# Performance work log

Hardware: AMD Instinct MI355X
Metric: run time of the kernel (lower is better)

## Reference

```python
import jax, jax.numpy as jnp
import numpy as np

NUM_USERS = 100000
NUM_ITEMS = 50000
EMBED_K = 64
N_EDGES = 2000000
N_NODES = NUM_USERS + NUM_ITEMS


def setup_inputs() -> dict:
    key = jax.random.key(0)
    k1, k2, k3, k4, k5 = jax.random.split(key, 5)
    # xavier_normal for [N, K]: std = sqrt(2 / (N + K)); use a simple small std
    def xav(k, n, d):
        std = np.sqrt(2.0 / (n + d)).astype(np.float32)
        return jax.random.normal(k, (n, d), dtype=jnp.float32) * std
    Gu = xav(k1, NUM_USERS, EMBED_K)
    Gi = xav(k2, NUM_ITEMS, EMBED_K)
    Gut = xav(k3, NUM_USERS, EMBED_K)
    Git = xav(k4, NUM_ITEMS, EMBED_K)
    edge_index = jax.random.randint(k5, (2, N_EDGES), 0, N_NODES, dtype=jnp.int32)
    return {"Gu": Gu, "Gi": Gi, "Gut": Gut, "Git": Git,
            "edge_index": edge_index, "n_layers": 3}


def reference(Gu, Gi, Gut, Git, edge_index, n_layers):
    n_nodes = Gu.shape[0] + Gi.shape[0]
    src, dst = edge_index[0], edge_index[1]
    # symmetric gcn normalization: 1/sqrt(deg_src * deg_dst)
    ones = jnp.ones(src.shape[0], dtype=Gu.dtype)
    deg = jax.ops.segment_sum(ones, dst, num_segments=n_nodes)
    deg = jnp.maximum(deg, 1.0)
    norm = jax.lax.rsqrt(deg[src] * deg[dst])  # [E]

    def prop(x):  # x: [N, K] -> [N, K]
        msg = x[src] * norm[:, None]           # [E, K] gather
        return jax.ops.segment_sum(msg, dst, num_segments=n_nodes)

    alpha = jnp.asarray([1.0 / (k + 1) for k in range(n_layers + 1)], dtype=Gu.dtype)

    def run(x0):
        out = alpha[0] * x0
        x = x0
        for k in range(n_layers):
            x = prop(x)
            out = out + alpha[k + 1] * x
        return out

    collab = run(jnp.concatenate([Gu, Gi], axis=0))   # LGConv stack
    textual = run(jnp.concatenate([Gut, Git], axis=0))  # NodeNodeTextLayer stack
    return collab + textual  # [N_NODES, K]
```

## Files before the change

### kernel.cpp

```cpp
#include <hip/hip_runtime.h>
#include <hip/hip_fp16.h>

#define KD 64
#define NPC 1024
#define TILE 2048

__device__ __forceinline__ float h2f(unsigned short u) {
    return __half2float(__ushort_as_half(u));
}
__device__ __forceinline__ unsigned short f2h(float f) {
    return __half_as_ushort(__float2half(f));
}


__global__ void bhist_kernel(const int* __restrict__ dst, int* __restrict__ cntb,
                             int E, int NBC) {
    extern __shared__ int lcnt[];
    for (int i = threadIdx.x; i < NBC; i += blockDim.x) lcnt[i] = 0;
    __syncthreads();
    for (int i = blockIdx.x * blockDim.x + threadIdx.x; i < E; i += gridDim.x * blockDim.x)
        atomicAdd(&lcnt[dst[i] >> 10], 1);
    __syncthreads();
    for (int i = threadIdx.x; i < NBC; i += blockDim.x) {
        int v = lcnt[i];
        if (v) atomicAdd(&cntb[i], v);
    }
}

__global__ void scan_small_kernel(const int* __restrict__ cnt, int* __restrict__ bptr,
                                  int* __restrict__ cursor, int n, int E) {
    __shared__ int s[256];
    int t = threadIdx.x;
    int v = (t < n) ? cnt[t] : 0;
    s[t] = v;
    __syncthreads();
    for (int off = 1; off < 256; off <<= 1) {
        int add = (t >= off) ? s[t - off] : 0;
        __syncthreads();
        s[t] += add;
        __syncthreads();
    }
    int excl = s[t] - v;
    if (t < n) { bptr[t] = excl; cursor[t] = excl; }
    if (t == 0) bptr[n] = E;
}


__global__ __launch_bounds__(256)
void csplit_kernel(const int* __restrict__ src, const int* __restrict__ dst,
                   int* __restrict__ cursor, unsigned int* __restrict__ staged,
                   int E, int NBC, int ntiles) {
    __shared__ unsigned int  ord[TILE];
    __shared__ unsigned short obkt[TILE];
    __shared__ int hist[256];
    __shared__ int lofs[256];
    __shared__ int gbase[256];
    int tid = threadIdx.x;

    for (int tile = blockIdx.x; tile < ntiles; tile += gridDim.x) {
        int e0 = tile * TILE;
        int n = E - e0; if (n > TILE) n = TILE;

        if (tid < NBC) hist[tid] = 0;
        __syncthreads();
        for (int i = tid; i < n; i += 256)
            atomicAdd(&hist[dst[e0 + i] >> 10], 1);
        __syncthreads();
        int v = (tid < NBC) ? hist[tid] : 0;
        lofs[tid] = v;
        __syncthreads();
        for (int off = 1; off < 256; off <<= 1) {
            int add = (tid >= off) ? lofs[tid - off] : 0;
            __syncthreads();
            lofs[tid] += add;
            __syncthreads();
        }
        int excl = lofs[tid] - v;
        lofs[tid] = excl;
        if (tid < NBC) {
            gbase[tid] = atomicAdd(&cursor[tid], v);
            hist[tid] = 0;
        }
        __syncthreads();
        for (int i = tid; i < n; i += 256) {
            int dd = dst[e0 + i];
            int ss = src[e0 + i];
            int b = dd >> 10;
            int p = lofs[b] + atomicAdd(&hist[b], 1);
            ord[p] = (unsigned int)ss | (((unsigned int)dd & 1023u) << 18);
            obkt[p] = (unsigned short)b;
        }
        __syncthreads();
        for (int i = tid; i < n; i += 256) {
            int b = obkt[i];
            staged[gbase[b] + (i - lofs[b])] = ord[i];
        }
        __syncthreads();
    }
}


__global__ __launch_bounds__(1024)
void csort_kernel(const unsigned int* __restrict__ staged, const int* __restrict__ bptr,
                  int* __restrict__ sorted_src, int2* __restrict__ rowinfo,
                  float* __restrict__ r, float* __restrict__ rinv,
                  int n_nodes, int E) {
    __shared__ int cnt[NPC];
    __shared__ int s[NPC];
    __shared__ int lofs[NPC];
    int b = blockIdx.x;
    int tid = threadIdx.x;
    int begin = bptr[b], end = bptr[b + 1];

    cnt[tid] = 0;
    __syncthreads();
    for (int i = begin + tid; i < end; i += 1024)
        atomicAdd(&cnt[(staged[i] >> 18) & 1023u], 1);
    __syncthreads();
    int v = cnt[tid];
    s[tid] = v;
    __syncthreads();
    for (int off = 1; off < 1024; off <<= 1) {
        int add = (tid >= off) ? s[tid - off] : 0;
        __syncthreads();
        s[tid] += add;
        __syncthreads();
    }
    int excl = s[tid] - v;
    lofs[tid] = excl;
    int node = b * NPC + tid;
    if (node < n_nodes) {
        float d = fmaxf((float)v, 1.0f);
        rowinfo[node] = make_int2(begin + excl, v);
        r[node] = rsqrtf(d);
        rinv[node] = sqrtf(d);
    }
    cnt[tid] = 0;
    __syncthreads();
    for (int i = begin + tid; i < end; i += 1024) {
        unsigned int u = staged[i];
        int ld = (u >> 18) & 1023u;
        int p = begin + lofs[ld] + atomicAdd(&cnt[ld], 1);
        sorted_src[p] = (int)(u & 0x3FFFFu);
    }
}


__global__ void combine_kernel(const float4* __restrict__ Gu, const float4* __restrict__ Gi,
                               const float4* __restrict__ Gut, const float4* __restrict__ Git,
                               const float* __restrict__ r,
                               ushort4* __restrict__ xs,
                               int nu4, int total4) {
    for (int i = blockIdx.x * blockDim.x + threadIdx.x; i < total4; i += gridDim.x * blockDim.x) {
        float4 a, b;
        if (i < nu4) { a = Gu[i]; b = Gut[i]; }
        else         { a = Gi[i - nu4]; b = Git[i - nu4]; }
        float rr = r[i >> 4];
        ushort4 p;
        p.x = f2h((a.x + b.x) * rr); p.y = f2h((a.y + b.y) * rr);
        p.z = f2h((a.z + b.z) * rr); p.w = f2h((a.w + b.w) * rr);
        xs[i] = p;
    }
}

__global__ __launch_bounds__(256)
void gather_kernel(const int2* __restrict__ rowinfo, const int* __restrict__ sorted_src,
                   const float* __restrict__ r, const uint2* __restrict__ xs,
                   ushort4* __restrict__ xs_next,
                   const float4* __restrict__ Gu, const float4* __restrict__ Gi,
                   const float4* __restrict__ Gut, const float4* __restrict__ Git,
                   const float* __restrict__ rinv,
                   const ushort4* __restrict__ xs1, const ushort4* __restrict__ xs2,
                   float4* __restrict__ out, int nu, int N, int zrow, int last) {
    int wid = (blockIdx.x * blockDim.x + threadIdx.x) >> 6;
    int lane = threadIdx.x & 63;
    int n0 = wid * 2;
    int n1 = n0 + 1;
    if (n0 >= N) return;
    int2 ri0 = rowinfo[n0];
    int2 ri1 = (n1 < N) ? rowinfo[n1] : make_int2(0, 0);
    int sub = lane >> 4;
    int li  = lane & 15;

    float ax0 = 0.f, ay0 = 0.f, az0 = 0.f, aw0 = 0.f;
    float ax1 = 0.f, ay1 = 0.f, az1 = 0.f, aw1 = 0.f;
    int maxy = ri0.y > ri1.y ? ri0.y : ri1.y;

    for (int boff = 0; boff < maxy; boff += 64) {
        int nb0 = ri0.y - boff; nb0 = nb0 < 0 ? 0 : (nb0 > 64 ? 64 : nb0);
        int nb1 = ri1.y - boff; nb1 = nb1 < 0 ? 0 : (nb1 > 64 ? 64 : nb1);
        int es0 = 0, es1 = 0;
        if (nb0 > 0) {
            int e = ri0.x + boff + lane;
            int laste = ri0.x + ri0.y - 1;
            es0 = sorted_src[e > laste ? laste : e];
        }
        if (nb1 > 0) {
            int e = ri1.x + boff + lane;
            int laste = ri1.x + ri1.y - 1;
            es1 = sorted_src[e > laste ? laste : e];
        }
        int nbm = nb0 > nb1 ? nb0 : nb1;
        for (int c = 0; c < nbm; c += 16) {
            int j0 = c + sub * 4;
            int t0 = __shfl(es0, j0 + 0);
            int t1 = __shfl(es0, j0 + 1);
            int t2 = __shfl(es0, j0 + 2);
            int t3 = __shfl(es0, j0 + 3);
            int q0 = __shfl(es1, j0 + 0);
            int q1 = __shfl(es1, j0 + 1);
            int q2 = __shfl(es1, j0 + 2);
            int q3 = __shfl(es1, j0 + 3);
            t0 = (j0     < nb0) ? t0 : zrow;
            t1 = (j0 + 1 < nb0) ? t1 : zrow;
            t2 = (j0 + 2 < nb0) ? t2 : zrow;
            t3 = (j0 + 3 < nb0) ? t3 : zrow;
            q0 = (j0     < nb1) ? q0 : zrow;
            q1 = (j0 + 1 < nb1) ? q1 : zrow;
            q2 = (j0 + 2 < nb1) ? q2 : zrow;
            q3 = (j0 + 3 < nb1) ? q3 : zrow;
            uint2 w0 = xs[t0 * 16 + li];
            uint2 w1 = xs[t1 * 16 + li];
            uint2 w2 = xs[t2 * 16 + li];
            uint2 w3 = xs[t3 * 16 + li];
            uint2 v0 = xs[q0 * 16 + li];
            uint2 v1 = xs[q1 * 16 + li];
            uint2 v2 = xs[q2 * 16 + li];
            uint2 v3 = xs[q3 * 16 + li];
            {
                __half2 sa = __hadd2(__hadd2(__builtin_bit_cast(__half2, w0.x),
                                             __builtin_bit_cast(__half2, w1.x)),
                                     __hadd2(__builtin_bit_cast(__half2, w2.x),
                                             __builtin_bit_cast(__half2, w3.x)));
                __half2 sb = __hadd2(__hadd2(__builtin_bit_cast(__half2, w0.y),
                                             __builtin_bit_cast(__half2, w1.y)),
                                     __hadd2(__builtin_bit_cast(__half2, w2.y),
                                             __builtin_bit_cast(__half2, w3.y)));
                float2 fa = __half22float2(sa);
                float2 fb = __half22float2(sb);
                ax0 += fa.x; ay0 += fa.y; az0 += fb.x; aw0 += fb.y;
            }
            {
                __half2 sa = __hadd2(__hadd2(__builtin_bit_cast(__half2, v0.x),
                                             __builtin_bit_cast(__half2, v1.x)),
                                     __hadd2(__builtin_bit_cast(__half2, v2.x),
                                             __builtin_bit_cast(__half2, v3.x)));
                __half2 sb = __hadd2(__hadd2(__builtin_bit_cast(__half2, v0.y),
                                             __builtin_bit_cast(__half2, v1.y)),
                                     __hadd2(__builtin_bit_cast(__half2, v2.y),
                                             __builtin_bit_cast(__half2, v3.y)));
                float2 fa = __half22float2(sa);
                float2 fb = __half22float2(sb);
                ax1 += fa.x; ay1 += fa.y; az1 += fb.x; aw1 += fb.y;
            }
        }
    }
    ax0 += __shfl_xor(ax0, 16); ay0 += __shfl_xor(ay0, 16);
    az0 += __shfl_xor(az0, 16); aw0 += __shfl_xor(aw0, 16);
    ax1 += __shfl_xor(ax1, 16); ay1 += __shfl_xor(ay1, 16);
    az1 += __shfl_xor(az1, 16); aw1 += __shfl_xor(aw1, 16);
    ax0 += __shfl_xor(ax0, 32); ay0 += __shfl_xor(ay0, 32);
    az0 += __shfl_xor(az0, 32); aw0 += __shfl_xor(aw0, 32);
    ax1 += __shfl_xor(ax1, 32); ay1 += __shfl_xor(ay1, 32);
    az1 += __shfl_xor(az1, 32); aw1 += __shfl_xor(aw1, 32);

    int node = (lane < 16) ? n0 : n1;
    int lli  = lane & 15;
    if (lane < 32 && node < N) {
        float sx = (lane < 16) ? ax0 : ax1;
        float sy = (lane < 16) ? ay0 : ay1;
        float sz = (lane < 16) ? az0 : az1;
        float sw = (lane < 16) ? aw0 : aw1;
        float rr = r[node];
        int idx = node * 16 + lli;
        if (!last) {
            float s = rr * rr;
            ushort4 p;
            p.x = f2h(sx * s); p.y = f2h(sy * s);
            p.z = f2h(sz * s); p.w = f2h(sw * s);
            xs_next[idx] = p;
        } else {
            const float a1 = 0.5f, a2 = 1.0f / 3.0f, a3 = 0.25f;
            float4 a, b;
            if (node < nu) { a = Gu[idx]; b = Gut[idx]; }
            else           { int j = idx - nu * 16; a = Gi[j]; b = Git[j]; }
            float rv = rinv[node];
            ushort4 u1 = xs1[idx];
            ushort4 u2 = xs2[idx];
            float4 o;
            o.x = a.x + b.x + rv * (a1 * h2f(u1.x) + a2 * h2f(u2.x)) + a3 * (sx * rr);
            o.y = a.y + b.y + rv * (a1 * h2f(u1.y) + a2 * h2f(u2.y)) + a3 * (sy * rr);
            o.z = a.z + b.z + rv * (a1 * h2f(u1.z) + a2 * h2f(u2.z)) + a3 * (sz * rr);
            o.w = a.w + b.w + rv * (a1 * h2f(u1.w) + a2 * h2f(u2.w)) + a3 * (sw * rr);
            out[idx] = o;
        }
    }
}


extern "C" void kernel_launch(void* const* d_in, const int* in_sizes, int n_in,
                              void* d_out, int out_size, void* d_ws, size_t ws_size,
                              hipStream_t stream) {
    const float* Gu  = (const float*)d_in[0];
    const float* Gi  = (const float*)d_in[1];
    const float* Gut = (const float*)d_in[2];
    const float* Git = (const float*)d_in[3];
    const int*   edge_index = (const int*)d_in[4];

    const int nuK = in_sizes[0];
    const int niK = in_sizes[1];
    const int n_nodes = (nuK + niK) / KD;
    const int E = in_sizes[4] / 2;
    const int totalK = nuK + niK;
    const int total4 = totalK / 4;
    const int nu4 = nuK / 4;
    const int nu = nuK / KD;
    const int NBC = (n_nodes + NPC - 1) / NPC;
    const int ntiles = (E + TILE - 1) / TILE;

    const int* src = edge_index;
    const int* dst = edge_index + E;

    auto align_up = [](size_t v) { return (v + 255) & ~(size_t)255; };
    char* ws = (char*)d_ws;
    size_t off = 0;
    int*          cntb       = (int*)(ws + off);          off += align_up((size_t)NBC * 4);
    int*          bptr       = (int*)(ws + off);          off += align_up((size_t)(NBC + 1) * 4);
    int*          cursor     = (int*)(ws + off);          off += align_up((size_t)NBC * 4);
    int2*         rowinfo    = (int2*)(ws + off);         off += align_up((size_t)n_nodes * 8);
    float*        r          = (float*)(ws + off);        off += align_up((size_t)n_nodes * 4);
    float*        rinv       = (float*)(ws + off);        off += align_up((size_t)n_nodes * 4);
    unsigned int* staged     = (unsigned int*)(ws + off); off += align_up((size_t)E * 4);
    int*          sorted_src = (int*)(ws + off);          off += align_up((size_t)E * 4);
    unsigned short* xs0      = (unsigned short*)(ws + off); off += align_up(((size_t)totalK + KD) * 2);
    unsigned short* xs1      = (unsigned short*)(ws + off); off += align_up(((size_t)totalK + KD) * 2);
    unsigned short* xs2      = (unsigned short*)(ws + off); off += align_up(((size_t)totalK + KD) * 2);
    if (off > ws_size) return;

    float* out = (float*)d_out;

    const int BLK = 256;
    const int grid_v = 2048;
    const int n_waves = (n_nodes + 1) / 2;
    const int grid_g = ((size_t)n_waves * 64 + BLK - 1) / BLK;
    const int zrow = n_nodes;

    hipMemsetAsync(cntb, 0, (size_t)NBC * 4, stream);
    hipMemsetAsync(xs0 + (size_t)n_nodes * KD, 0, KD * 2, stream);
    hipMemsetAsync(xs1 + (size_t)n_nodes * KD, 0, KD * 2, stream);
    hipMemsetAsync(xs2 + (size_t)n_nodes * KD, 0, KD * 2, stream);

    bhist_kernel<<<256, BLK, (size_t)NBC * 4, stream>>>(dst, cntb, E, NBC);
    scan_small_kernel<<<1, 256, 0, stream>>>(cntb, bptr, cursor, NBC, E);
    csplit_kernel<<<ntiles, BLK, 0, stream>>>(src, dst, cursor, staged, E, NBC, ntiles);
    csort_kernel<<<NBC, 1024, 0, stream>>>(staged, bptr, sorted_src, rowinfo, r, rinv,
                                           n_nodes, E);

    combine_kernel<<<grid_v, BLK, 0, stream>>>((const float4*)Gu, (const float4*)Gi,
                                               (const float4*)Gut, (const float4*)Git,
                                               r, (ushort4*)xs0, nu4, total4);

    gather_kernel<<<grid_g, BLK, 0, stream>>>(rowinfo, sorted_src, r,
                                              (const uint2*)xs0, (ushort4*)xs1,
                                              nullptr, nullptr, nullptr, nullptr,
                                              nullptr, nullptr, nullptr, nullptr,
                                              nu, n_nodes, zrow, 0);
    gather_kernel<<<grid_g, BLK, 0, stream>>>(rowinfo, sorted_src, r,
                                              (const uint2*)xs1, (ushort4*)xs2,
                                              nullptr, nullptr, nullptr, nullptr,
                                              nullptr, nullptr, nullptr, nullptr,
                                              nu, n_nodes, zrow, 0);
    gather_kernel<<<grid_g, BLK, 0, stream>>>(rowinfo, sorted_src, r,
                                              (const uint2*)xs2, nullptr,
                                              (const float4*)Gu, (const float4*)Gi,
                                              (const float4*)Gut, (const float4*)Git,
                                              rinv, (const ushort4*)xs1,
                                              (const ushort4*)xs2,
                                              (float4*)out, nu, n_nodes, zrow, 1);
}
```

Baseline: 230.6 us.

## Map four nodes per wavefront with one 16-lane group per node in gather

The gather kernel now gives each wavefront four destination nodes, each served by one 16-lane group that reads its own 16 neighbor ids per step, instead of two nodes spread across all four subgroups. This removes the cross-subgroup shuffle reductions at the end and halves the number of waves launched. In exchange each wave runs to the longest of four degrees rather than two, so divergence from imbalanced degrees may grow. Each group still issues four gathers per inner step.

```diff
diff --git a/kernel.cpp b/kernel.cpp
--- a/kernel.cpp
+++ b/kernel.cpp
@@ -174,110 +174,56 @@
                    float4* __restrict__ out, int nu, int N, int zrow, int last) {
     int wid = (blockIdx.x * blockDim.x + threadIdx.x) >> 6;
     int lane = threadIdx.x & 63;
-    int n0 = wid * 2;
-    int n1 = n0 + 1;
-    if (n0 >= N) return;
-    int2 ri0 = rowinfo[n0];
-    int2 ri1 = (n1 < N) ? rowinfo[n1] : make_int2(0, 0);
     int sub = lane >> 4;
     int li  = lane & 15;
-
-    float ax0 = 0.f, ay0 = 0.f, az0 = 0.f, aw0 = 0.f;
-    float ax1 = 0.f, ay1 = 0.f, az1 = 0.f, aw1 = 0.f;
-    int maxy = ri0.y > ri1.y ? ri0.y : ri1.y;
-
-    for (int boff = 0; boff < maxy; boff += 64) {
-        int nb0 = ri0.y - boff; nb0 = nb0 < 0 ? 0 : (nb0 > 64 ? 64 : nb0);
-        int nb1 = ri1.y - boff; nb1 = nb1 < 0 ? 0 : (nb1 > 64 ? 64 : nb1);
-        int es0 = 0, es1 = 0;
-        if (nb0 > 0) {
-            int e = ri0.x + boff + lane;
-            int laste = ri0.x + ri0.y - 1;
-            es0 = sorted_src[e > laste ? laste : e];
-        }
-        if (nb1 > 0) {
-            int e = ri1.x + boff + lane;
-            int laste = ri1.x + ri1.y - 1;
-            es1 = sorted_src[e > laste ? laste : e];
-        }
-        int nbm = nb0 > nb1 ? nb0 : nb1;
-        for (int c = 0; c < nbm; c += 16) {
-            int j0 = c + sub * 4;
-            int t0 = __shfl(es0, j0 + 0);
-            int t1 = __shfl(es0, j0 + 1);
-            int t2 = __shfl(es0, j0 + 2);
-            int t3 = __shfl(es0, j0 + 3);
-            int q0 = __shfl(es1, j0 + 0);
-            int q1 = __shfl(es1, j0 + 1);
-            int q2 = __shfl(es1, j0 + 2);
-            int q3 = __shfl(es1, j0 + 3);
-            t0 = (j0     < nb0) ? t0 : zrow;
-            t1 = (j0 + 1 < nb0) ? t1 : zrow;
-            t2 = (j0 + 2 < nb0) ? t2 : zrow;
-            t3 = (j0 + 3 < nb0) ? t3 : zrow;
-            q0 = (j0     < nb1) ? q0 : zrow;
-            q1 = (j0 + 1 < nb1) ? q1 : zrow;
-            q2 = (j0 + 2 < nb1) ? q2 : zrow;
-            q3 = (j0 + 3 < nb1) ? q3 : zrow;
+    int node = wid * 4 + sub;
+    if (wid * 4 >= N) return;
+    int2 ri = (node < N) ? rowinfo[node] : make_int2(0, 0);
+
+    int maxy = ri.y;
+    maxy = max(maxy, __shfl_xor(maxy, 16));
+    maxy = max(maxy, __shfl_xor(maxy, 32));
+
+    float ax = 0.f, ay = 0.f, az = 0.f, aw = 0.f;
+    int lastp = ri.x + (ri.y > 0 ? ri.y - 1 : 0);
+
+    for (int boff = 0; boff < maxy; boff += 16) {
+        int e = ri.x + boff + li;
+        int id = sorted_src[e > lastp ? lastp : e];
+        id = (boff + li < ri.y) ? id : zrow;
+#pragma unroll
+        for (int c = 0; c < 16; c += 4) {
+            int sl = (sub << 4) + c;
+            int t0 = __shfl(id, sl + 0);
+            int t1 = __shfl(id, sl + 1);
+            int t2 = __shfl(id, sl + 2);
+            int t3 = __shfl(id, sl + 3);
             uint2 w0 = xs[t0 * 16 + li];
             uint2 w1 = xs[t1 * 16 + li];
             uint2 w2 = xs[t2 * 16 + li];
             uint2 w3 = xs[t3 * 16 + li];
-            uint2 v0 = xs[q0 * 16 + li];
-            uint2 v1 = xs[q1 * 16 + li];
-            uint2 v2 = xs[q2 * 16 + li];
-            uint2 v3 = xs[q3 * 16 + li];
-            {
-                __half2 sa = __hadd2(__hadd2(__builtin_bit_cast(__half2, w0.x),
-                                             __builtin_bit_cast(__half2, w1.x)),
-                                     __hadd2(__builtin_bit_cast(__half2, w2.x),
-                                             __builtin_bit_cast(__half2, w3.x)));
-                __half2 sb = __hadd2(__hadd2(__builtin_bit_cast(__half2, w0.y),
-                                             __builtin_bit_cast(__half2, w1.y)),
-                                     __hadd2(__builtin_bit_cast(__half2, w2.y),
-                                             __builtin_bit_cast(__half2, w3.y)));
-                float2 fa = __half22float2(sa);
-                float2 fb = __half22float2(sb);
-                ax0 += fa.x; ay0 += fa.y; az0 += fb.x; aw0 += fb.y;
-            }
-            {
-                __half2 sa = __hadd2(__hadd2(__builtin_bit_cast(__half2, v0.x),
-                                             __builtin_bit_cast(__half2, v1.x)),
-                                     __hadd2(__builtin_bit_cast(__half2, v2.x),
-                                             __builtin_bit_cast(__half2, v3.x)));
-                __half2 sb = __hadd2(__hadd2(__builtin_bit_cast(__half2, v0.y),
-                                             __builtin_bit_cast(__half2, v1.y)),
-                                     __hadd2(__builtin_bit_cast(__half2, v2.y),
-                                             __builtin_bit_cast(__half2, v3.y)));
-                float2 fa = __half22float2(sa);
-                float2 fb = __half22float2(sb);
-                ax1 += fa.x; ay1 += fa.y; az1 += fb.x; aw1 += fb.y;
-            }
-        }
-    }
-    ax0 += __shfl_xor(ax0, 16); ay0 += __shfl_xor(ay0, 16);
-    az0 += __shfl_xor(az0, 16); aw0 += __shfl_xor(aw0, 16);
-    ax1 += __shfl_xor(ax1, 16); ay1 += __shfl_xor(ay1, 16);
-    az1 += __shfl_xor(az1, 16); aw1 += __shfl_xor(aw1, 16);
-    ax0 += __shfl_xor(ax0, 32); ay0 += __shfl_xor(ay0, 32);
-    az0 += __shfl_xor(az0, 32); aw0 += __shfl_xor(aw0, 32);
-    ax1 += __shfl_xor(ax1, 32); ay1 += __shfl_xor(ay1, 32);
-    az1 += __shfl_xor(az1, 32); aw1 += __shfl_xor(aw1, 32);
-
-    int node = (lane < 16) ? n0 : n1;
-    int lli  = lane & 15;
-    if (lane < 32 && node < N) {
-        float sx = (lane < 16) ? ax0 : ax1;
-        float sy = (lane < 16) ? ay0 : ay1;
-        float sz = (lane < 16) ? az0 : az1;
-        float sw = (lane < 16) ? aw0 : aw1;
+            __half2 sa = __hadd2(__hadd2(__builtin_bit_cast(__half2, w0.x),
+                                         __builtin_bit_cast(__half2, w1.x)),
+                                 __hadd2(__builtin_bit_cast(__half2, w2.x),
+                                         __builtin_bit_cast(__half2, w3.x)));
+            __half2 sb = __hadd2(__hadd2(__builtin_bit_cast(__half2, w0.y),
+                                         __builtin_bit_cast(__half2, w1.y)),
+                                 __hadd2(__builtin_bit_cast(__half2, w2.y),
+                                         __builtin_bit_cast(__half2, w3.y)));
+            float2 fa = __half22float2(sa);
+            float2 fb = __half22float2(sb);
+            ax += fa.x; ay += fa.y; az += fb.x; aw += fb.y;
+        }
+    }
+
+    if (node < N) {
         float rr = r[node];
-        int idx = node * 16 + lli;
+        int idx = node * 16 + li;
         if (!last) {
             float s = rr * rr;
             ushort4 p;
-            p.x = f2h(sx * s); p.y = f2h(sy * s);
-            p.z = f2h(sz * s); p.w = f2h(sw * s);
+            p.x = f2h(ax * s); p.y = f2h(ay * s);
+            p.z = f2h(az * s); p.w = f2h(aw * s);
             xs_next[idx] = p;
         } else {
             const float a1 = 0.5f, a2 = 1.0f / 3.0f, a3 = 0.25f;
@@ -288,10 +234,10 @@
             ushort4 u1 = xs1[idx];
             ushort4 u2 = xs2[idx];
             float4 o;
-            o.x = a.x + b.x + rv * (a1 * h2f(u1.x) + a2 * h2f(u2.x)) + a3 * (sx * rr);
-            o.y = a.y + b.y + rv * (a1 * h2f(u1.y) + a2 * h2f(u2.y)) + a3 * (sy * rr);
-            o.z = a.z + b.z + rv * (a1 * h2f(u1.z) + a2 * h2f(u2.z)) + a3 * (sz * rr);
-            o.w = a.w + b.w + rv * (a1 * h2f(u1.w) + a2 * h2f(u2.w)) + a3 * (sw * rr);
+            o.x = a.x + b.x + rv * (a1 * h2f(u1.x) + a2 * h2f(u2.x)) + a3 * (ax * rr);
+            o.y = a.y + b.y + rv * (a1 * h2f(u1.y) + a2 * h2f(u2.y)) + a3 * (ay * rr);
+            o.z = a.z + b.z + rv * (a1 * h2f(u1.z) + a2 * h2f(u2.z)) + a3 * (az * rr);
+            o.w = a.w + b.w + rv * (a1 * h2f(u1.w) + a2 * h2f(u2.w)) + a3 * (aw * rr);
             out[idx] = o;
         }
     }
@@ -341,7 +287,7 @@
 
     const int BLK = 256;
     const int grid_v = 2048;
-    const int n_waves = (n_nodes + 1) / 2;
+    const int n_waves = (n_nodes + 3) / 4;
     const int grid_g = ((size_t)n_waves * 64 + BLK - 1) / BLK;
     const int zrow = n_nodes;
 
```

Measured after the change: 224.8 us. -2.5%, faster.
